# Kernel tuning notes

Measured on AMD Instinct MI355X. Metric: run time of the kernel, lower is better.

Reference implementation:

```python
import jax, jax.numpy as jnp
import numpy as np

WEIGHT = 1.0  # init kwarg: loss weight
N = 4096
D_FEAT = 128


def _pairwise_dist(x):
    # x: [n, d] -> D: [n, n] Euclidean distances (safe sqrt for grad at 0)
    sq = jnp.sum(x * x, axis=-1)
    d2 = sq[:, None] + sq[None, :] - 2.0 * (x @ x.T)
    d2 = jnp.maximum(d2, 0.0)
    pos = d2 > 1e-12
    return jnp.where(pos, jnp.sqrt(jnp.where(pos, d2, 1.0)), 0.0)


def _prim_mst(D):
    # Vectorized Prim: returns (parents, children) of the n-1 MST edges.
    # filtration value (VR complex truncated at max_dimension=1).
    n = D.shape[0]
    INF = jnp.finfo(D.dtype).max
    visited0 = jnp.zeros(n, dtype=bool).at[0].set(True)
    mind0 = D[0]
    parent0 = jnp.zeros(n, dtype=jnp.int32)

    def step(carry, _):
        visited, mind, parent = carry
        j = jnp.argmin(jnp.where(visited, INF, mind))
        pj = parent[j]
        visited = visited.at[j].set(True)
        better = (D[j] < mind) & (~visited)
        mind = jnp.where(better, D[j], mind)
        parent = jnp.where(better, j, parent)
        return (visited, mind, parent), (pj, j.astype(jnp.int32))

    _, (pjs, js) = jax.lax.scan(step, (visited0, mind0, parent0), None, length=n - 1)
    return pjs, js


def _h1_persistence(x):
    # H1 diagram for VR complex with max_dimension=1: a 1-cycle is born when a
    # non-MST edge appears; with no 2-simplices it never dies, so deaths are
    # capped at the maximal filtration value. Persistence = cap - birth.
    n = x.shape[0]
    D = _pairwise_dist(x)
    pjs, js = _prim_mst(D)
    tree = jnp.zeros((n, n), dtype=bool)
    tree = tree.at[pjs, js].set(True)
    tree = tree | tree.T
    iu = np.triu_indices(n, 1)  # static indices
    births = D[iu]              # [n*(n-1)/2]
    is_tree = tree[iu]
    cap = jnp.max(D)
    # tree edges are H0 (not H1): give them zero persistence (diagonal points)
    return jnp.where(is_tree, 0.0, cap - births)


def _wasserstein_1d(p1, p2):
    # 1-Wasserstein between equal-size persistence multisets via sorted matching
    # (deaths share a common cap per diagram, so matching by sorted persistence).
    return jnp.sum(jnp.abs(jnp.sort(p1) - jnp.sort(p2)))


def setup_inputs() -> dict:
    key = jax.random.key(0)
    k1, k2, k3, k4 = jax.random.split(key, 4)
    return {
        "graph1_features": jax.random.normal(k1, (N, D_FEAT), dtype=jnp.float32),
        "graph1_edges": jax.random.randint(k2, (2, 8 * N), 0, N, dtype=jnp.int64),
        "graph2_features": jax.random.normal(k3, (N, D_FEAT), dtype=jnp.float32),
        "graph2_edges": jax.random.randint(k4, (2, 8 * N), 0, N, dtype=jnp.int64),
    }


def reference(graph1_features, graph1_edges, graph2_features, graph2_edges):
    # edge tensors are unused: the torch forward builds VR complexes from the
    # point clouds only (build_from_points), matching the original module.
    p1 = _h1_persistence(graph1_features)
    p2 = _h1_persistence(graph2_features)
    return WEIGHT * _wasserstein_1d(p1, p2)
```

## Files before the change

kernel.cpp:

```cpp
#include <hip/hip_runtime.h>
#include <stdint.h>

#define NN 4096
#define DF 128
#define NBINS 16384
#define NSLAB 256
#define BORUVKA_ROUNDS 12

typedef __attribute__((ext_vector_type(8))) short short8;
typedef __attribute__((ext_vector_type(4))) float floatx4;
typedef __attribute__((ext_vector_type(4))) unsigned short ushort4_t;
typedef __attribute__((ext_vector_type(4))) int int4_t;

__device__ __forceinline__ unsigned bin_of(float v, float scale) {
  if (v < 0.f) v = 0.f;
  unsigned b = (unsigned)(v * scale);
  return b >= (unsigned)NBINS ? (unsigned)(NBINS - 1) : b;
}

__global__ void k_rownorm(const float* __restrict__ x1, const float* __restrict__ x2,
                          float* __restrict__ sq) {
  int i = blockIdx.x * blockDim.x + threadIdx.x;
  if (i >= 2 * NN) return;
  const float* x = (i < NN) ? x1 : x2;
  int r = i & (NN - 1);
  const float* row = x + (size_t)r * DF;
  float s = 0.f;
  for (int k = 0; k < DF; ++k) s += row[k] * row[k];
  sq[i] = s;
}

__global__ __launch_bounds__(256) void k_bound(const float* __restrict__ sq,
                                               float* __restrict__ hdrf) {
  int t = threadIdx.x;
  float m = 0.f;
  for (int i = t; i < 2 * NN; i += 256) m = fmaxf(m, sq[i]);
  for (int off = 32; off > 0; off >>= 1) m = fmaxf(m, __shfl_down(m, off, 64));
  __shared__ float wm[4];
  if ((t & 63) == 0) wm[t >> 6] = m;
  __syncthreads();
  if (t == 0) {
    float mm = fmaxf(fmaxf(wm[0], wm[1]), fmaxf(wm[2], wm[3]));
    float dbound = 2.f * sqrtf(mm);
    hdrf[2] = 65535.f / dbound;
    hdrf[3] = dbound / 65535.f;
  }
}

__global__ void k_split(const float* __restrict__ x1, const float* __restrict__ x2,
                        unsigned short* __restrict__ xh, unsigned short* __restrict__ xl) {
  int i = blockIdx.x * blockDim.x + threadIdx.x;
  if (i >= 2 * NN * DF) return;
  const float* x = (i < NN * DF) ? x1 : x2;
  float v = x[i & (NN * DF - 1)];
  unsigned u = __float_as_uint(v);
  unsigned hu = u & 0xffff0000u;
  float hf = __uint_as_float(hu);
  float lf = v - hf;
  unsigned lu = __float_as_uint(lf) & 0xffff0000u;
  xh[i] = (unsigned short)(hu >> 16);
  xl[i] = (unsigned short)(lu >> 16);
}

__global__ __launch_bounds__(256) void k_dist(const unsigned short* __restrict__ Xhi,
                                              const unsigned short* __restrict__ Xlo,
                                              const float* __restrict__ sq,
                                              const float* __restrict__ hdrf,
                                              unsigned short* __restrict__ Qbase,
                                              unsigned* __restrict__ caps) {
  int bi = blockIdx.y, bj = blockIdx.x;
  if (bi > bj) return;
  bool offdiag = (bi != bj);
  int g = blockIdx.z;
  const unsigned short* xh = Xhi + (size_t)g * NN * DF;
  const unsigned short* xl = Xlo + (size_t)g * NN * DF;
  const float* sqg = sq + g * NN;
  unsigned short* Q = Qbase + (size_t)g * NN * NN;
  float qs = hdrf[2];
  int t = threadIdx.x;
  int w = t >> 6, lane = t & 63;
  int m = lane & 15, quad = lane >> 4;
  int i0 = bi * 128 + (w >> 1) * 64;
  int j0 = bj * 128 + (w & 1) * 64;
  floatx4 acc[4][4];
#pragma unroll
  for (int ti = 0; ti < 4; ++ti)
#pragma unroll
    for (int tj = 0; tj < 4; ++tj) acc[ti][tj] = (floatx4){0.f, 0.f, 0.f, 0.f};
#pragma unroll
  for (int kc = 0; kc < DF; kc += 32) {
    short8 ah[4], al[4], bh[4], bl[4];
#pragma unroll
    for (int ti = 0; ti < 4; ++ti) {
      size_t ra = (size_t)(i0 + ti * 16 + m) * DF + kc + quad * 8;
      size_t rb = (size_t)(j0 + ti * 16 + m) * DF + kc + quad * 8;
      ah[ti] = *(const short8*)&xh[ra];
      al[ti] = *(const short8*)&xl[ra];
      bh[ti] = *(const short8*)&xh[rb];
      bl[ti] = *(const short8*)&xl[rb];
    }
#pragma unroll
    for (int ti = 0; ti < 4; ++ti)
#pragma unroll
      for (int tj = 0; tj < 4; ++tj) {
        acc[ti][tj] = __builtin_amdgcn_mfma_f32_16x16x32_bf16(ah[ti], bh[tj], acc[ti][tj], 0, 0, 0);
        acc[ti][tj] = __builtin_amdgcn_mfma_f32_16x16x32_bf16(ah[ti], bl[tj], acc[ti][tj], 0, 0, 0);
        acc[ti][tj] = __builtin_amdgcn_mfma_f32_16x16x32_bf16(al[ti], bh[tj], acc[ti][tj], 0, 0, 0);
      }
  }
  float sqj[4];
#pragma unroll
  for (int tj = 0; tj < 4; ++tj) sqj[tj] = sqg[j0 + tj * 16 + m];
  float mx = 0.f;
#pragma unroll
  for (int ti = 0; ti < 4; ++ti) {
    int ib = i0 + ti * 16 + quad * 4;
    float sqiv[4];
#pragma unroll
    for (int r = 0; r < 4; ++r) sqiv[r] = sqg[ib + r];
#pragma unroll
    for (int tj = 0; tj < 4; ++tj) {
      int jj = j0 + tj * 16 + m;
      ushort4_t qv;
#pragma unroll
      for (int r = 0; r < 4; ++r) {
        float d2 = sqiv[r] + sqj[tj] - 2.f * acc[ti][tj][r];
        d2 = fmaxf(d2, 0.f);
        float d = (d2 > 1e-12f) ? sqrtf(d2) : 0.f;
        mx = fmaxf(mx, d);
        unsigned q = (unsigned)(d * qs + 0.5f);
        if (q > 65535u) q = 65535u;
        qv[r] = (unsigned short)q;
      }
      *(ushort4_t*)&Q[(size_t)jj * NN + ib] = qv;
      if (offdiag) {
#pragma unroll
        for (int r = 0; r < 4; ++r) Q[(size_t)(ib + r) * NN + jj] = qv[r];
      }
    }
  }
  for (int off = 32; off > 0; off >>= 1) mx = fmaxf(mx, __shfl_down(mx, off, 64));
  __shared__ float wmax[4];
  if (lane == 0) wmax[w] = mx;
  __syncthreads();
  if (t == 0) {
    float mm = fmaxf(fmaxf(wmax[0], wmax[1]), fmaxf(wmax[2], wmax[3]));
    atomicMax(&caps[g], __float_as_uint(mm));
  }
}

__global__ void k_binit(int* __restrict__ comp, unsigned long long* __restrict__ compbest,
                        unsigned long long* __restrict__ bestkey,
                        int* __restrict__ mstcnt, int* __restrict__ ncomp) {
  int i = blockIdx.x * blockDim.x + threadIdx.x;
  if (i >= 2 * NN) return;
  comp[i] = i & (NN - 1);
  compbest[i] = ~0ull;
  bestkey[i] = ~0ull;
  if ((i & (NN - 1)) == 0) {
    mstcnt[i >> 12] = 0;
    ncomp[i >> 12] = NN;
  }
}

__global__ __launch_bounds__(256) void k_minedge(const unsigned short* __restrict__ Qbase,
                                                 const int* __restrict__ comp_base,
                                                 unsigned long long* __restrict__ compbest_base,
                                                 unsigned long long* __restrict__ bestkey_base,
                                                 const int* __restrict__ ncomp) {
  int g = blockIdx.y;
  if (ncomp[g] == 1) return;
  int w = threadIdx.x >> 6, lane = threadIdx.x & 63;
  int v = blockIdx.x * 4 + w;
  const int* comp = comp_base + g * NN;
  unsigned long long* cbest = compbest_base + (size_t)g * NN;
  unsigned long long* bkp = bestkey_base + (size_t)g * NN;
  int cv = comp[v];
  unsigned long long bk = bkp[v];
  if (bk != ~0ull) {
    int bj = (int)(bk & 0xfffull);
    if (comp[bj] != cv) {
      if (lane == 0) atomicMin(&cbest[cv], bk);
      return;
    }
  }
  const unsigned short* row = Qbase + ((size_t)g * NN + (size_t)v) * NN;
  unsigned long long best = ~0ull;
#pragma unroll 4
  for (int it = 0; it < NN / 256; ++it) {
    int jb = (it * 64 + lane) * 4;
    ushort4_t rw = *(const ushort4_t*)&row[jb];
    int4_t cj = *(const int4_t*)&comp[jb];
#pragma unroll
    for (int u = 0; u < 4; ++u) {
      if (cj[u] != cv) {
        unsigned long long key = ((unsigned long long)rw[u] << 24) |
                                 ((unsigned long long)v << 12) | (unsigned)(jb + u);
        if (key < best) best = key;
      }
    }
  }
  for (int off = 32; off > 0; off >>= 1) {
    unsigned long long o = __shfl_down(best, off, 64);
    if (o < best) best = o;
  }
  if (lane == 0) {
    bkp[v] = best;
    if (best != ~0ull) atomicMin(&cbest[cv], best);
  }
}

__global__ __launch_bounds__(512) void k_hook(unsigned long long* __restrict__ compbest_base,
                                              int* __restrict__ comp_base,
                                              const float* __restrict__ hdrf,
                                              float* __restrict__ mstw_base,
                                              int* __restrict__ mstcnt,
                                              int* __restrict__ ncomp) {
  int g = blockIdx.x;
  if (ncomp[g] == 1) return;
  unsigned long long* cb = compbest_base + (size_t)g * NN;
  int* comp = comp_base + g * NN;
  float* mstw = mstw_base + g * (NN - 1);
  float qinv = hdrf[3];
  __shared__ int par[NN];
  __shared__ unsigned char live[NN];
  __shared__ int newcnt;
  int t = threadIdx.x;
  if (t == 0) newcnt = 0;
  for (int c = t; c < NN; c += 512) {
    unsigned long long key = cb[c];
    bool a = (key != ~0ull);
    live[c] = a ? 1 : 0;
    int p = c;
    if (a) {
      int j = (int)(key & 0xfffull);
      p = comp[j];
    }
    par[c] = p;
  }
  __syncthreads();
  for (int c = t; c < NN; c += 512) {
    int p = par[c];
    if (p != c && par[p] == c && c < p) par[c] = c;
  }
  __syncthreads();
  for (int c = t; c < NN; c += 512) {
    if (live[c] && par[c] != c) {
      float w = (float)((unsigned)(cb[c] >> 24)) * qinv;
      int slot = atomicAdd(&mstcnt[g], 1);
      mstw[slot] = w;
    }
  }
  __syncthreads();
  for (;;) {
    int np[NN / 512];
    bool ch = false;
    int k = 0;
    for (int c = t; c < NN; c += 512, ++k) {
      int p = par[c];
      int pp = par[p];
      np[k] = pp;
      if (pp != p) ch = true;
    }
    __syncthreads();
    k = 0;
    for (int c = t; c < NN; c += 512, ++k) par[c] = np[k];
    if (!__syncthreads_or(ch)) break;
  }
  int cnt = 0;
  for (int c = t; c < NN; c += 512)
    if (live[c] && par[c] == c) cnt++;
  for (int off = 32; off > 0; off >>= 1) cnt += __shfl_down(cnt, off, 64);
  if ((t & 63) == 0 && cnt) atomicAdd(&newcnt, cnt);
  for (int v = t; v < NN; v += 512) comp[v] = par[comp[v]];
  for (int c = t; c < NN; c += 512) cb[c] = ~0ull;
  __syncthreads();
  if (t == 0) ncomp[g] = newcnt;
}

__global__ __launch_bounds__(256) void k_hist(const unsigned short* __restrict__ Qbase,
                                              const unsigned* __restrict__ caps,
                                              const float* __restrict__ hdrf,
                                              unsigned* __restrict__ Hs) {
  __shared__ unsigned h[NBINS];
  int t = threadIdx.x;
  for (int i = t; i < NBINS; i += 256) h[i] = 0;
  int b = blockIdx.x;
  int g = b >> 8, s = b & (NSLAB - 1);
  const unsigned short* Q = Qbase + (size_t)g * NN * NN;
  float cap = __uint_as_float(caps[g]);
  float capmax = fmaxf(__uint_as_float(caps[0]), __uint_as_float(caps[1]));
  float scale = (float)NBINS / capmax;
  float qinv = hdrf[3];
  __syncthreads();
  for (int p = s; p < NN / 2; p += NSLAB) {
    int r1 = p, r2 = NN - 1 - p;
    const unsigned short* row1 = Q + (size_t)r1 * NN;
    const unsigned short* row2 = Q + (size_t)r2 * NN;
    for (int j = r1 + 1 + t; j < NN; j += 256)
      atomicAdd(&h[bin_of(cap - (float)row1[j] * qinv, scale)], 1u);
    for (int j = r2 + 1 + t; j < NN; j += 256)
      atomicAdd(&h[bin_of(cap - (float)row2[j] * qinv, scale)], 1u);
  }
  __syncthreads();
  unsigned* slab = Hs + (size_t)b * NBINS;
  for (int i = t; i < NBINS; i += 256) slab[i] = h[i];
}

__global__ void k_treefix(const float* __restrict__ twbase, const unsigned* __restrict__ caps,
                          unsigned* __restrict__ Hs) {
  int g = blockIdx.y;
  unsigned* hist = Hs + (size_t)(g * NSLAB) * NBINS;
  float cap = __uint_as_float(caps[g]);
  float capmax = fmaxf(__uint_as_float(caps[0]), __uint_as_float(caps[1]));
  float scale = (float)NBINS / capmax;
  int idx = blockIdx.x * blockDim.x + threadIdx.x;
  if (idx < NN - 1) {
    float w = twbase[g * (NN - 1) + idx];
    atomicSub(&hist[bin_of(cap - w, scale)], 1u);
    atomicAdd(&hist[0], 1u);
  }
}

__global__ __launch_bounds__(256) void k_merge(const unsigned* __restrict__ Hs,
                                               unsigned* __restrict__ Hm) {
  int id = blockIdx.x * 256 + threadIdx.x;
  int g = id >> 14;
  int i = id & (NBINS - 1);
  const unsigned* base = Hs + (size_t)(g * NSLAB) * NBINS + i;
  unsigned sum = 0;
  for (int s = 0; s < NSLAB; ++s) sum += base[(size_t)s * NBINS];
  Hm[id] = sum;
}

__global__ __launch_bounds__(256) void k_w1(const unsigned* __restrict__ Hm,
                                            const unsigned* __restrict__ caps,
                                            float* __restrict__ out) {
  int t = threadIdx.x;
  const int PB = NBINS / 256;
  int base = t * PB;
  long long tsum = 0;
  for (int i = 0; i < PB; ++i)
    tsum += (long long)(int)(Hm[base + i] - Hm[NBINS + base + i]);
  int lane = t & 63, wid = t >> 6;
  long long incl = tsum;
  for (int off = 1; off < 64; off <<= 1) {
    long long o = __shfl_up(incl, off, 64);
    if (lane >= off) incl += o;
  }
  __shared__ long long wtot[4];
  if (lane == 63) wtot[wid] = incl;
  __syncthreads();
  long long run = incl - tsum;
  for (int w = 0; w < wid; ++w) run += wtot[w];
  unsigned long long local = 0;
  for (int i = 0; i < PB; ++i) {
    run += (long long)(int)(Hm[base + i] - Hm[NBINS + base + i]);
    local += (unsigned long long)(run < 0 ? -run : run);
  }
  for (int off = 32; off > 0; off >>= 1) local += __shfl_down(local, off, 64);
  __shared__ unsigned long long wl[4];
  if (lane == 0) wl[wid] = local;
  __syncthreads();
  if (t == 0) {
    float capmax = fmaxf(__uint_as_float(caps[0]), __uint_as_float(caps[1]));
    double dt = (double)capmax / (double)NBINS;
    out[0] = (float)((double)(wl[0] + wl[1] + wl[2] + wl[3]) * dt);
  }
}

__global__ void k_fail(float* out) { out[0] = -1234567.0f; }

extern "C" void kernel_launch(void* const* d_in, const int* in_sizes, int n_in,
                              void* d_out, int out_size, void* d_ws, size_t ws_size,
                              hipStream_t stream) {
  const float* x1 = (const float*)d_in[0];
  const float* x2 = (const float*)d_in[2];
  float* out = (float*)d_out;
  char* ws = (char*)d_ws;

  const size_t offQ = 0;
  const size_t offS = 2ull * NN * NN * 2ull;
  const size_t offHm = offS + 2ull * NSLAB * NBINS * 4ull;
  const size_t offHdr = offHm + 2ull * NBINS * 4ull;
  const size_t offSq = offHdr + 64;
  const size_t offTw = offSq + 2ull * NN * 4ull;
  const size_t offCb = (offTw + 2ull * (NN - 1) * 4ull + 7ull) & ~7ull;
  const size_t offBk = offCb + 2ull * NN * 8ull;
  const size_t offCp = offBk + 2ull * NN * 8ull;
  const size_t offMeta = offCp + 2ull * NN * 4ull;
  const size_t needed = offMeta + 64;
  if (ws_size < needed) {
    hipLaunchKernelGGL(k_fail, dim3(1), dim3(1), 0, stream, out);
    return;
  }

  unsigned short* Qbase = (unsigned short*)(ws + offQ);
  unsigned* Hs = (unsigned*)(ws + offS);
  unsigned short* Xhi = (unsigned short*)(ws + offS);
  unsigned short* Xlo = (unsigned short*)(ws + offS + 2ull * NN * DF * 2ull);
  unsigned* Hm = (unsigned*)(ws + offHm);
  unsigned* caps = (unsigned*)(ws + offHdr);
  float* hdrf = (float*)(ws + offHdr);
  float* sq = (float*)(ws + offSq);
  float* tw = (float*)(ws + offTw);
  unsigned long long* compbest = (unsigned long long*)(ws + offCb);
  unsigned long long* bestkey = (unsigned long long*)(ws + offBk);
  int* comp = (int*)(ws + offCp);
  int* mstcnt = (int*)(ws + offMeta);
  int* ncomp = (int*)(ws + offMeta + 8);

  hipMemsetAsync(ws + offHdr, 0, 64, stream);

  hipLaunchKernelGGL(k_rownorm, dim3((2 * NN + 255) / 256), dim3(256), 0, stream, x1, x2, sq);
  hipLaunchKernelGGL(k_bound, dim3(1), dim3(256), 0, stream, sq, hdrf);
  hipLaunchKernelGGL(k_split, dim3((2 * NN * DF + 255) / 256), dim3(256), 0, stream,
                     x1, x2, Xhi, Xlo);
  hipLaunchKernelGGL(k_dist, dim3(NN / 128, NN / 128, 2), dim3(256), 0, stream,
                     Xhi, Xlo, sq, hdrf, Qbase, caps);
  hipLaunchKernelGGL(k_binit, dim3((2 * NN + 255) / 256), dim3(256), 0, stream,
                     comp, compbest, bestkey, mstcnt, ncomp);
  for (int r = 0; r < BORUVKA_ROUNDS; ++r) {
    hipLaunchKernelGGL(k_minedge, dim3(NN / 4, 2), dim3(256), 0, stream,
                       Qbase, comp, compbest, bestkey, ncomp);
    hipLaunchKernelGGL(k_hook, dim3(2), dim3(512), 0, stream,
                       compbest, comp, hdrf, tw, mstcnt, ncomp);
  }
  hipLaunchKernelGGL(k_hist, dim3(2 * NSLAB), dim3(256), 0, stream, Qbase, caps, hdrf, Hs);
  hipLaunchKernelGGL(k_treefix, dim3(16, 2), dim3(256), 0, stream, tw, caps, Hs);
  hipLaunchKernelGGL(k_merge, dim3(2 * NBINS / 256), dim3(256), 0, stream, Hs, Hm);
  hipLaunchKernelGGL(k_w1, dim3(1), dim3(256), 0, stream, Hm, caps, out);
}
```

Baseline: 412.8 us.

## Precompute per-segment row minima to skip full row scans in Boruvka

Adds a kernel that, once after the distance matrix is built, stores the minimum quantized distance and its offset for each 64-column segment of every row. In each Boruvka round a lane first checks its segment minimum. If that edge leaves the vertex's component it is used directly, and the lane rescans its segment only when the minimum is internal. This replaces repeated full reads of Q and comp across rounds with one extra full pass plus a 2MB segment table. Lanes now read contiguous 64-element chunks instead of interleaved ones, which makes the rescan loads strided across lanes.

```diff
diff --git a/kernel.cpp b/kernel.cpp
--- a/kernel.cpp
+++ b/kernel.cpp
@@ -6,6 +6,7 @@
 #define NBINS 16384
 #define NSLAB 256
 #define BORUVKA_ROUNDS 12
+#define NSEG 64
 
 typedef __attribute__((ext_vector_type(8))) short short8;
 typedef __attribute__((ext_vector_type(4))) float floatx4;
@@ -149,6 +150,26 @@
   }
 }
 
+__global__ __launch_bounds__(256) void k_segmin(const unsigned short* __restrict__ Qbase,
+                                                unsigned* __restrict__ Sbase) {
+  int g = blockIdx.y;
+  int w = threadIdx.x >> 6, lane = threadIdx.x & 63;
+  int v = blockIdx.x * 4 + w;
+  const unsigned short* row = Qbase + ((size_t)g * NN + (size_t)v) * NN;
+  unsigned best = 0xffffffffu;
+#pragma unroll 4
+  for (int k = 0; k < 16; ++k) {
+    int jb = lane * 64 + k * 4;
+    ushort4_t rw = *(const ushort4_t*)&row[jb];
+#pragma unroll
+    for (int u = 0; u < 4; ++u) {
+      unsigned key = ((unsigned)rw[u] << 6) | (unsigned)(k * 4 + u);
+      if (key < best) best = key;
+    }
+  }
+  Sbase[((size_t)g * NN + v) * NSEG + lane] = best;
+}
+
 __global__ void k_binit(int* __restrict__ comp, unsigned long long* __restrict__ compbest,
                         unsigned long long* __restrict__ bestkey,
                         int* __restrict__ mstcnt, int* __restrict__ ncomp) {
@@ -164,6 +185,7 @@
 }
 
 __global__ __launch_bounds__(256) void k_minedge(const unsigned short* __restrict__ Qbase,
+                                                 const unsigned* __restrict__ Sbase,
                                                  const int* __restrict__ comp_base,
                                                  unsigned long long* __restrict__ compbest_base,
                                                  unsigned long long* __restrict__ bestkey_base,
@@ -184,19 +206,26 @@
       return;
     }
   }
-  const unsigned short* row = Qbase + ((size_t)g * NN + (size_t)v) * NN;
+  unsigned skey = Sbase[((size_t)g * NN + v) * NSEG + lane];
+  int sj = lane * 64 + (int)(skey & 63u);
   unsigned long long best = ~0ull;
+  if (comp[sj] != cv) {
+    best = ((unsigned long long)(skey >> 6) << 24) |
+           ((unsigned long long)v << 12) | (unsigned)sj;
+  } else {
+    const unsigned short* row = Qbase + ((size_t)g * NN + (size_t)v) * NN;
 #pragma unroll 4
-  for (int it = 0; it < NN / 256; ++it) {
-    int jb = (it * 64 + lane) * 4;
-    ushort4_t rw = *(const ushort4_t*)&row[jb];
-    int4_t cj = *(const int4_t*)&comp[jb];
-#pragma unroll
-    for (int u = 0; u < 4; ++u) {
-      if (cj[u] != cv) {
-        unsigned long long key = ((unsigned long long)rw[u] << 24) |
-                                 ((unsigned long long)v << 12) | (unsigned)(jb + u);
-        if (key < best) best = key;
+    for (int k = 0; k < 16; ++k) {
+      int jb = lane * 64 + k * 4;
+      ushort4_t rw = *(const ushort4_t*)&row[jb];
+      int4_t cj = *(const int4_t*)&comp[jb];
+#pragma unroll
+      for (int u = 0; u < 4; ++u) {
+        if (cj[u] != cv) {
+          unsigned long long key = ((unsigned long long)rw[u] << 24) |
+                                   ((unsigned long long)v << 12) | (unsigned)(jb + u);
+          if (key < best) best = key;
+        }
       }
     }
   }
@@ -389,7 +418,8 @@
   const size_t offBk = offCb + 2ull * NN * 8ull;
   const size_t offCp = offBk + 2ull * NN * 8ull;
   const size_t offMeta = offCp + 2ull * NN * 4ull;
-  const size_t needed = offMeta + 64;
+  const size_t offSeg = offMeta + 64;
+  const size_t needed = offSeg + 2ull * NN * NSEG * 4ull;
   if (ws_size < needed) {
     hipLaunchKernelGGL(k_fail, dim3(1), dim3(1), 0, stream, out);
     return;
@@ -409,6 +439,7 @@
   int* comp = (int*)(ws + offCp);
   int* mstcnt = (int*)(ws + offMeta);
   int* ncomp = (int*)(ws + offMeta + 8);
+  unsigned* Sbase = (unsigned*)(ws + offSeg);
 
   hipMemsetAsync(ws + offHdr, 0, 64, stream);
 
@@ -418,11 +449,12 @@
                      x1, x2, Xhi, Xlo);
   hipLaunchKernelGGL(k_dist, dim3(NN / 128, NN / 128, 2), dim3(256), 0, stream,
                      Xhi, Xlo, sq, hdrf, Qbase, caps);
+  hipLaunchKernelGGL(k_segmin, dim3(NN / 4, 2), dim3(256), 0, stream, Qbase, Sbase);
   hipLaunchKernelGGL(k_binit, dim3((2 * NN + 255) / 256), dim3(256), 0, stream,
                      comp, compbest, bestkey, mstcnt, ncomp);
   for (int r = 0; r < BORUVKA_ROUNDS; ++r) {
     hipLaunchKernelGGL(k_minedge, dim3(NN / 4, 2), dim3(256), 0, stream,
-                       Qbase, comp, compbest, bestkey, ncomp);
+                       Qbase, Sbase, comp, compbest, bestkey, ncomp);
     hipLaunchKernelGGL(k_hook, dim3(2), dim3(512), 0, stream,
                        compbest, comp, hdrf, tw, mstcnt, ncomp);
   }
```

After: 432.6 us. +4.8%, slower.

## Compute full distance matrix instead of mirroring upper triangle with scattered stores

Applied to the files above, without the earlier changes.

The distance kernel no longer skips lower-triangle tiles and mirrors each result with scalar 2-byte scattered stores. Every tile is now computed directly, with the MFMA operands swapped so each lane holds four consecutive columns of one row and writes them as a single 8-byte vector store. This removes the uncoalesced transposed writes at the cost of roughly doubling the MFMA work in the distance stage. The 3-term bf16 split is now applied asymmetrically, so mirrored entries may differ slightly in rounding.

```diff
diff --git a/kernel.cpp b/kernel.cpp
--- a/kernel.cpp
+++ b/kernel.cpp
@@ -68,9 +68,6 @@
                                               const float* __restrict__ hdrf,
                                               unsigned short* __restrict__ Qbase,
                                               unsigned* __restrict__ caps) {
-  int bi = blockIdx.y, bj = blockIdx.x;
-  if (bi > bj) return;
-  bool offdiag = (bi != bj);
   int g = blockIdx.z;
   const unsigned short* xh = Xhi + (size_t)g * NN * DF;
   const unsigned short* xl = Xlo + (size_t)g * NN * DF;
@@ -80,8 +77,8 @@
   int t = threadIdx.x;
   int w = t >> 6, lane = t & 63;
   int m = lane & 15, quad = lane >> 4;
-  int i0 = bi * 128 + (w >> 1) * 64;
-  int j0 = bj * 128 + (w & 1) * 64;
+  int i0 = blockIdx.y * 128 + (w >> 1) * 64;
+  int j0 = blockIdx.x * 128 + (w & 1) * 64;
   floatx4 acc[4][4];
 #pragma unroll
   for (int ti = 0; ti < 4; ++ti)
@@ -103,28 +100,26 @@
     for (int ti = 0; ti < 4; ++ti)
 #pragma unroll
       for (int tj = 0; tj < 4; ++tj) {
-        acc[ti][tj] = __builtin_amdgcn_mfma_f32_16x16x32_bf16(ah[ti], bh[tj], acc[ti][tj], 0, 0, 0);
-        acc[ti][tj] = __builtin_amdgcn_mfma_f32_16x16x32_bf16(ah[ti], bl[tj], acc[ti][tj], 0, 0, 0);
-        acc[ti][tj] = __builtin_amdgcn_mfma_f32_16x16x32_bf16(al[ti], bh[tj], acc[ti][tj], 0, 0, 0);
+        acc[ti][tj] = __builtin_amdgcn_mfma_f32_16x16x32_bf16(bh[tj], ah[ti], acc[ti][tj], 0, 0, 0);
+        acc[ti][tj] = __builtin_amdgcn_mfma_f32_16x16x32_bf16(bh[tj], al[ti], acc[ti][tj], 0, 0, 0);
+        acc[ti][tj] = __builtin_amdgcn_mfma_f32_16x16x32_bf16(bl[tj], ah[ti], acc[ti][tj], 0, 0, 0);
       }
   }
-  float sqj[4];
-#pragma unroll
-  for (int tj = 0; tj < 4; ++tj) sqj[tj] = sqg[j0 + tj * 16 + m];
   float mx = 0.f;
 #pragma unroll
   for (int ti = 0; ti < 4; ++ti) {
-    int ib = i0 + ti * 16 + quad * 4;
-    float sqiv[4];
-#pragma unroll
-    for (int r = 0; r < 4; ++r) sqiv[r] = sqg[ib + r];
+    int i = i0 + ti * 16 + m;
+    float sqi = sqg[i];
+    unsigned short* qrow = Q + (size_t)i * NN;
 #pragma unroll
     for (int tj = 0; tj < 4; ++tj) {
-      int jj = j0 + tj * 16 + m;
+      int jb = j0 + tj * 16 + quad * 4;
+      float4 sqjv = *(const float4*)&sqg[jb];
       ushort4_t qv;
 #pragma unroll
       for (int r = 0; r < 4; ++r) {
-        float d2 = sqiv[r] + sqj[tj] - 2.f * acc[ti][tj][r];
+        float sj = (r == 0) ? sqjv.x : (r == 1) ? sqjv.y : (r == 2) ? sqjv.z : sqjv.w;
+        float d2 = sqi + sj - 2.f * acc[ti][tj][r];
         d2 = fmaxf(d2, 0.f);
         float d = (d2 > 1e-12f) ? sqrtf(d2) : 0.f;
         mx = fmaxf(mx, d);
@@ -132,11 +127,7 @@
         if (q > 65535u) q = 65535u;
         qv[r] = (unsigned short)q;
       }
-      *(ushort4_t*)&Q[(size_t)jj * NN + ib] = qv;
-      if (offdiag) {
-#pragma unroll
-        for (int r = 0; r < 4; ++r) Q[(size_t)(ib + r) * NN + jj] = qv[r];
-      }
+      *(ushort4_t*)&qrow[jb] = qv;
     }
   }
   for (int off = 32; off > 0; off >>= 1) mx = fmaxf(mx, __shfl_down(mx, off, 64));
```

Result: slower. 432.1 us (+4.7%).
